# Performance work log

Hardware: AMD Instinct MI355X
Metric: run time of the kernel (lower is better)

Reference implementation:

```python
import jax, jax.numpy as jnp
import numpy as np

EMBED_DIM = 1024
NUM_HEADS = 16
HEAD_DIM = EMBED_DIM // NUM_HEADS


def setup_inputs() -> dict:
    key = jax.random.key(0)
    ks = jax.random.split(key, 9)
    B, S, E = 2, 2048, EMBED_DIM
    scale = 1.0 / np.sqrt(E)
    return {
        "query": jax.random.normal(ks[0], (B, S, E), jnp.float32),
        "key": jax.random.normal(ks[1], (B, S, E), jnp.float32),
        "value": jax.random.normal(ks[2], (B, S, E), jnp.float32),
        "wq": jax.random.normal(ks[3], (E, E), jnp.float32) * scale,
        "bq": jnp.zeros((E,), jnp.float32),
        "wk": jax.random.normal(ks[4], (E, E), jnp.float32) * scale,
        "bk": jnp.zeros((E,), jnp.float32),
        "wv": jax.random.normal(ks[5], (E, E), jnp.float32) * scale,
        "bv": jnp.zeros((E,), jnp.float32),
    }


def _split_heads(x):
    B, S, _ = x.shape
    return x.reshape(B, S, NUM_HEADS, HEAD_DIM).transpose(0, 2, 1, 3)  # [B,H,S,Dh]


def reference(query, key, value, wq, bq, wk, bk, wv, bv):
    q = _split_heads(query @ wq + bq)   # [B,H,S,Dh]
    k = _split_heads(key @ wk + bk)
    v = _split_heads(value @ wv + bv)
    logits = jnp.einsum("bhqd,bhkd->bhqk", q, k) / jnp.sqrt(
        jnp.asarray(HEAD_DIM, q.dtype)
    )
    attn = jax.nn.softmax(logits, axis=-1)          # [B,H,S,S]
    out = jnp.einsum("bhqk,bhkd->bhqd", attn, v)    # [B,H,S,Dh]
    B, H, S, Dh = out.shape
    out = out.transpose(0, 2, 1, 3).reshape(B, S, H * Dh)  # [B,S,E]
    return out, attn
```

## Files before the change

### kernel.cpp

```cpp
#include <hip/hip_runtime.h>

typedef float  f32x4   __attribute__((ext_vector_type(4)));
typedef float  f32x16  __attribute__((ext_vector_type(16)));
typedef int    i32x4   __attribute__((ext_vector_type(4)));
typedef short  bf16x8  __attribute__((ext_vector_type(8)));
typedef short  s16x4   __attribute__((ext_vector_type(4)));

#define NB   2
#define SEQ  2048
#define EMB  1024
#define NH   16
#define DH   64
#define MATN (NB * SEQ * EMB)

__device__ inline short f2bf(float f) {
    unsigned u = __float_as_uint(f);
    u += 0x7fffu + ((u >> 16) & 1u);
    return (short)(u >> 16);
}

__device__ inline unsigned cvtpk(float lo, float hi) {
    unsigned r;
    asm("v_cvt_pk_bf16_f32 %0, %1, %2" : "=v"(r) : "v"(lo), "v"(hi));
    return r;
}

__device__ inline float fexp2(float x) {
#if __has_builtin(__builtin_amdgcn_exp2f)
    return __builtin_amdgcn_exp2f(x);
#else
    return exp2f(x);
#endif
}

__device__ inline f32x4 mfma16(bf16x8 a, bf16x8 b, f32x4 c) {
    return __builtin_amdgcn_mfma_f32_16x16x32_bf16(a, b, c, 0, 0, 0);
}
__device__ inline f32x16 mfma32(bf16x8 a, bf16x8 b, f32x16 c) {
    return __builtin_amdgcn_mfma_f32_32x32x16_bf16(a, b, c, 0, 0, 0);
}

__device__ inline void gload_lds16(const short* g, short* l) {
    __builtin_amdgcn_global_load_lds(
        (const __attribute__((address_space(1))) void*)g,
        (__attribute__((address_space(3))) void*)l, 16, 0, 0);
}

__global__ __launch_bounds__(256) void prep_kernel(const float* __restrict__ q,
                                                   const float* __restrict__ k,
                                                   const float* __restrict__ v,
                                                   const float* __restrict__ w0,
                                                   const float* __restrict__ w1,
                                                   const float* __restrict__ w2,
                                                   short* __restrict__ wt,
                                                   short* __restrict__ abf) {
    int blk = blockIdx.x;
    int t = threadIdx.x;
    if (blk < 3072) {
        __shared__ float tile[32][33];
        int mat = blk >> 10;
        int rem = blk & 1023;
        int kt = rem >> 5, nt = rem & 31;
        const float* W = (mat == 0) ? w0 : ((mat == 1) ? w1 : w2);
        int row = t >> 3, c4 = (t & 7) << 2;

        f32x4 val = *(const f32x4*)(W + (kt * 32 + row) * EMB + nt * 32 + c4);
        tile[row][c4 + 0] = val[0];
        tile[row][c4 + 1] = val[1];
        tile[row][c4 + 2] = val[2];
        tile[row][c4 + 3] = val[3];
        __syncthreads();

        int n = nt * 32 + row;
        s16x4 o;
        o[0] = f2bf(tile[c4 + 0][row]);
        o[1] = f2bf(tile[c4 + 1][row]);
        o[2] = f2bf(tile[c4 + 2][row]);
        o[3] = f2bf(tile[c4 + 3][row]);
        *(s16x4*)(wt + mat * (EMB * EMB) + n * EMB + kt * 32 + c4) = o;
    } else {
        long long i = (long long)(blk - 3072) * 2048 + t * 8;
        int mat = (int)(i >> 22);
        int off = (int)(i & (MATN - 1));
        const float* A = (mat == 0) ? q : ((mat == 1) ? k : v);
        f32x4 x = *(const f32x4*)(A + off);
        f32x4 y = *(const f32x4*)(A + off + 4);
        bf16x8 pk;
        pk[0] = f2bf(x[0]); pk[1] = f2bf(x[1]); pk[2] = f2bf(x[2]); pk[3] = f2bf(x[3]);
        pk[4] = f2bf(y[0]); pk[5] = f2bf(y[1]); pk[6] = f2bf(y[2]); pk[7] = f2bf(y[3]);
        *(bf16x8*)(abf + i) = pk;
    }
}

template <bool BF16A>
__global__ __launch_bounds__(256) void proj_kernel(const short* __restrict__ abf,
                                                   const float* __restrict__ a0,
                                                   const float* __restrict__ a1,
                                                   const float* __restrict__ a2,
                                                   const float* __restrict__ b0,
                                                   const float* __restrict__ b1,
                                                   const float* __restrict__ b2,
                                                   const short* __restrict__ wt,
                                                   short* __restrict__ qkv) {
    __shared__ __align__(16) short smem[18432];

    int orig = blockIdx.x;
    int blk = (orig & 7) * 96 + (orig >> 3);
    int mat = blk >> 8;
    int rem = blk & 255;
    int mt = rem >> 3, nt = rem & 7;

    const float* bias = (mat == 0) ? b0 : ((mat == 1) ? b1 : b2);
    const float* Af = (mat == 0) ? a0 : ((mat == 1) ? a1 : a2);
    const short* Ab = abf + mat * MATN;
    const short* WT = wt + mat * (EMB * EMB);
    short* O = qkv + mat * MATN;
    float scale = (mat == 0) ? 0.125f * 1.44269504f : 1.0f;

    int t = threadIdx.x;
    int lane = t & 63, w = t >> 6;
    int wr = w >> 1, wc = w & 1;
    int lg = lane >> 4, lm = lane & 15;

    int m0 = mt * 128, n0 = nt * 128;

    f32x4 acc[4][4] = {};

    if constexpr (BF16A) {
        const short* gA[4];
        const short* gW[4];
        int ldso[4];
#pragma unroll
        for (int i = 0; i < 4; i++) {
            int u = w * 256 + i * 64 + lane;
            int row = u >> 3;
            int c = (u & 7) ^ (row & 7);
            gA[i] = Ab + (m0 + row) * EMB + c * 8;
            gW[i] = WT + (n0 + row) * EMB + c * 8;
            ldso[i] = (w * 256 + i * 64) * 8;
        }
        int xr = lm & 7;
        for (int k0 = 0; k0 < EMB; k0 += 64) {
#pragma unroll
            for (int i = 0; i < 4; i++) {
                gload_lds16(gA[i] + k0, smem + ldso[i]);
                gload_lds16(gW[i] + k0, smem + 8192 + ldso[i]);
            }
            __syncthreads();
#pragma unroll
            for (int ks = 0; ks < 2; ks++) {
                bf16x8 af[4], bfr[4];
                int cc = (ks * 4 + lg) ^ xr;
#pragma unroll
                for (int mi = 0; mi < 4; mi++)
                    af[mi] = *(const bf16x8*)(smem + (wr * 64 + mi * 16 + lm) * 64 + cc * 8);
#pragma unroll
                for (int ni = 0; ni < 4; ni++)
                    bfr[ni] = *(const bf16x8*)(smem + 8192 + (wc * 64 + ni * 16 + lm) * 64 + cc * 8);
#pragma unroll
                for (int mi = 0; mi < 4; mi++)
#pragma unroll
                    for (int ni = 0; ni < 4; ni++)
                        acc[mi][ni] = mfma16(af[mi], bfr[ni], acc[mi][ni]);
            }
            __syncthreads();
        }
    } else {
        int srow = t >> 1, koff = (t & 1) * 32;
        for (int k0 = 0; k0 < EMB; k0 += 64) {
            const float* ap = Af + (m0 + srow) * EMB + k0 + koff;
#pragma unroll
            for (int i = 0; i < 4; i++) {
                f32x4 x = *(const f32x4*)(ap + i * 8);
                f32x4 y = *(const f32x4*)(ap + i * 8 + 4);
                bf16x8 pk;
                pk[0] = f2bf(x[0]); pk[1] = f2bf(x[1]); pk[2] = f2bf(x[2]); pk[3] = f2bf(x[3]);
                pk[4] = f2bf(y[0]); pk[5] = f2bf(y[1]); pk[6] = f2bf(y[2]); pk[7] = f2bf(y[3]);
                *(bf16x8*)&smem[srow * 72 + koff + i * 8] = pk;
            }
            const short* wp = WT + (n0 + srow) * EMB + k0 + koff;
#pragma unroll
            for (int i = 0; i < 4; i++)
                *(i32x4*)&smem[9216 + srow * 72 + koff + i * 8] = *(const i32x4*)(wp + i * 8);
            __syncthreads();
#pragma unroll
            for (int ks = 0; ks < 2; ks++) {
                bf16x8 af[4], bfr[4];
#pragma unroll
                for (int mi = 0; mi < 4; mi++)
                    af[mi] = *(const bf16x8*)&smem[(wr * 64 + mi * 16 + lm) * 72 + ks * 32 + lg * 8];
#pragma unroll
                for (int ni = 0; ni < 4; ni++)
                    bfr[ni] = *(const bf16x8*)&smem[9216 + (wc * 64 + ni * 16 + lm) * 72 + ks * 32 + lg * 8];
#pragma unroll
                for (int mi = 0; mi < 4; mi++)
#pragma unroll
                    for (int ni = 0; ni < 4; ni++)
                        acc[mi][ni] = mfma16(af[mi], bfr[ni], acc[mi][ni]);
            }
            __syncthreads();
        }
    }

    int bidx = m0 >> 11;
    if (mat == 2) {
#pragma unroll
        for (int ni = 0; ni < 4; ni++) {
            int e = n0 + wc * 64 + ni * 16 + lm;
            float bv = bias[e];
            int h = e >> 6, d = e & 63;
#pragma unroll
            for (int mi = 0; mi < 4; mi++) {
                int s = (m0 + wr * 64 + mi * 16 + lg * 4) & (SEQ - 1);
                s16x4 o;
#pragma unroll
                for (int r = 0; r < 4; r++) o[r] = f2bf(acc[mi][ni][r] + bv);
                *(s16x4*)(O + (((bidx * NH + h) * DH + d) * SEQ) + s) = o;
            }
        }
    } else {
#pragma unroll
        for (int ni = 0; ni < 4; ni++) {
            int e = n0 + wc * 64 + ni * 16 + lm;
            float bv = bias[e];
#pragma unroll
            for (int mi = 0; mi < 4; mi++) {
                int rr = wr * 64 + mi * 16 + lg * 4;
#pragma unroll
                for (int r = 0; r < 4; r++)
                    smem[(rr + r) * 136 + wc * 64 + ni * 16 + lm] =
                        f2bf((acc[mi][ni][r] + bv) * scale);
            }
        }
        __syncthreads();
        int r = t >> 1, half = t & 1;
        int h = (n0 + half * 64) >> 6;
        int s = (m0 + r) & (SEQ - 1);
        short* dst = O + (((long long)bidx * NH + h) * SEQ + s) * DH;
        const short* srcp = smem + r * 136 + half * 64;
#pragma unroll
        for (int j = 0; j < 8; j++)
            *(i32x4*)(dst + j * 8) = *(const i32x4*)(srcp + j * 8);
    }
}

__global__ __launch_bounds__(256) void attn_kernel(const short* __restrict__ qkv,
                                                   float* __restrict__ out,
                                                   float* __restrict__ attn) {
    const short* Qb = qkv;
    const short* Kb = qkv + MATN;
    const short* Vt = qkv + 2 * MATN;

    __shared__ __align__(16) short kbuf[2][64][72];
    __shared__ __align__(16) short vbuf[2][4096];
    __shared__ float lds_rs[4][32];

    int orig = blockIdx.x;
    int wg = (orig & 7) * 128 + (orig >> 3);
    int bh = wg >> 5;
    int q0 = (wg & 31) * 64;
    int b = bh >> 4, hq = bh & 15;

    int t = threadIdx.x, lane = t & 63, w = t >> 6;
    int srow = t >> 2, sch = t & 3;
    int l31 = lane & 31, l5 = lane >> 5;
    int qh = w & 1, kh = w >> 1;

    const short* kbase = Kb + (long long)bh * SEQ * DH;
    const short* vbase = Vt + (long long)bh * DH * SEQ;

    bf16x8 qw[4];
    {
        const short* qr = Qb + ((long long)bh * SEQ + q0 + qh * 32 + l31) * DH + l5 * 8;
        qw[0] = *(const bf16x8*)(qr);
        qw[1] = *(const bf16x8*)(qr + 16);
        qw[2] = *(const bf16x8*)(qr + 32);
        qw[3] = *(const bf16x8*)(qr + 48);
    }

    i32x4 kr0, kr1;
    {
        const short* kp = kbase + srow * DH + sch * 16;
        kr0 = *(const i32x4*)(kp); kr1 = *(const i32x4*)(kp + 8);
    }
    float rsum = 0.0f;
    for (int kt = 0; kt < 32; kt++) {
        *(i32x4*)&kbuf[kt & 1][srow][sch * 16]     = kr0;
        *(i32x4*)&kbuf[kt & 1][srow][sch * 16 + 8] = kr1;
        __syncthreads();
        if (kt < 31) {
            const short* kp = kbase + ((kt + 1) * 64 + srow) * DH + sch * 16;
            kr0 = *(const i32x4*)(kp); kr1 = *(const i32x4*)(kp + 8);
        }
        const short* kb = &kbuf[kt & 1][kh * 32 + l31][l5 * 8];
        f32x16 s = {};
        __builtin_amdgcn_s_setprio(1);
        s = mfma32(*(const bf16x8*)(kb),      qw[0], s);
        s = mfma32(*(const bf16x8*)(kb + 16), qw[1], s);
        s = mfma32(*(const bf16x8*)(kb + 32), qw[2], s);
        s = mfma32(*(const bf16x8*)(kb + 48), qw[3], s);
        __builtin_amdgcn_s_setprio(0);
#pragma unroll
        for (int r = 0; r < 16; r++) rsum += fexp2(s[r]);
    }
    rsum += __shfl_xor(rsum, 32);
    if (lane < 32) lds_rs[w][lane] = rsum;
    __syncthreads();
    float ml2r = -__log2f(lds_rs[qh][l31] + lds_rs[2 + qh][l31]);

    f32x16 acc2[2] = {};
    float* arow2 = attn + ((long long)bh * SEQ + q0 + qh * 32 + l31) * SEQ + kh * 32;

    int vidx = ((sch >> 1) * 2 + (sch & 1)) * 2 + (srow >> 5);
    int vA = vidx * 512 + (srow & 31) * 8;

    i32x4 vr0, vr1;
    {
        const short* kp = kbase + srow * DH + sch * 16;
        kr0 = *(const i32x4*)(kp); kr1 = *(const i32x4*)(kp + 8);
        const short* vp = vbase + srow * SEQ + sch * 16;
        vr0 = *(const i32x4*)(vp); vr1 = *(const i32x4*)(vp + 8);
    }

    for (int kt = 0; kt < 32; kt++) {
        *(i32x4*)&kbuf[kt & 1][srow][sch * 16]     = kr0;
        *(i32x4*)&kbuf[kt & 1][srow][sch * 16 + 8] = kr1;
        union { i32x4 v; s16x4 h[2]; } u0, u1;
        u0.v = vr0; u1.v = vr1;
        *(s16x4*)&vbuf[kt & 1][vA]       = u0.h[0];
        *(s16x4*)&vbuf[kt & 1][vA + 256] = u0.h[1];
        *(s16x4*)&vbuf[kt & 1][vA + 4]   = u1.h[0];
        *(s16x4*)&vbuf[kt & 1][vA + 260] = u1.h[1];
        __syncthreads();
        if (kt < 31) {
            const short* kp = kbase + ((kt + 1) * 64 + srow) * DH + sch * 16;
            kr0 = *(const i32x4*)(kp); kr1 = *(const i32x4*)(kp + 8);
            const short* vp = vbase + srow * SEQ + (kt + 1) * 64 + sch * 16;
            vr0 = *(const i32x4*)(vp); vr1 = *(const i32x4*)(vp + 8);
        }

        const short* kb2 = &kbuf[kt & 1][kh * 32 + l31][l5 * 8];
        f32x16 s;
#pragma unroll
        for (int r = 0; r < 16; r++) s[r] = ml2r;
        __builtin_amdgcn_s_setprio(1);
        s = mfma32(*(const bf16x8*)(kb2),      qw[0], s);
        s = mfma32(*(const bf16x8*)(kb2 + 16), qw[1], s);
        s = mfma32(*(const bf16x8*)(kb2 + 32), qw[2], s);
        s = mfma32(*(const bf16x8*)(kb2 + 48), qw[3], s);
        __builtin_amdgcn_s_setprio(0);

        float p[16];
#pragma unroll
        for (int rg = 0; rg < 4; rg++) {
            f32x4 st;
#pragma unroll
            for (int j = 0; j < 4; j++) {
                float e = fexp2(s[rg * 4 + j]);
                p[rg * 4 + j] = e;
                st[j] = e;
            }
            *(f32x4*)(arow2 + kt * 64 + rg * 8 + l5 * 4) = st;
        }

        bf16x8 pb[2];
#pragma unroll
        for (int c = 0; c < 2; c++) {
            union { unsigned d[4]; bf16x8 v; } up;
            up.d[0] = cvtpk(p[c * 8 + 0], p[c * 8 + 1]);
            up.d[1] = cvtpk(p[c * 8 + 2], p[c * 8 + 3]);
            up.d[2] = cvtpk(p[c * 8 + 4], p[c * 8 + 5]);
            up.d[3] = cvtpk(p[c * 8 + 6], p[c * 8 + 7]);
            pb[c] = up.v;
        }

        __builtin_amdgcn_s_setprio(1);
#pragma unroll
        for (int db = 0; db < 2; db++) {
#pragma unroll
            for (int c = 0; c < 2; c++) {
                bf16x8 vf = *(const bf16x8*)&vbuf[kt & 1]
                    [((kh * 2 + c) * 2 + db) * 512 + l5 * 256 + l31 * 8];
                acc2[db] = mfma32(vf, pb[c], acc2[db]);
            }
        }
        __builtin_amdgcn_s_setprio(0);
    }

    __syncthreads();
    float* mrg = (float*)&kbuf[0][0][0];
    if (kh == 1) {
#pragma unroll
        for (int db = 0; db < 2; db++)
#pragma unroll
            for (int rg = 0; rg < 4; rg++) {
                f32x4 v = {acc2[db][rg * 4 + 0], acc2[db][rg * 4 + 1],
                           acc2[db][rg * 4 + 2], acc2[db][rg * 4 + 3]};
                *(f32x4*)&mrg[((qh * 2 + db) * 4 + rg) * 256 + lane * 4] = v;
            }
    }
    __syncthreads();
    if (kh == 0) {
        float* op2 = out + ((long long)b * SEQ + q0 + qh * 32 + l31) * EMB + hq * DH;
#pragma unroll
        for (int db = 0; db < 2; db++)
#pragma unroll
            for (int rg = 0; rg < 4; rg++) {
                f32x4 m = *(const f32x4*)&mrg[((qh * 2 + db) * 4 + rg) * 256 + lane * 4];
                f32x4 o = {acc2[db][rg * 4 + 0] + m[0], acc2[db][rg * 4 + 1] + m[1],
                           acc2[db][rg * 4 + 2] + m[2], acc2[db][rg * 4 + 3] + m[3]};
                *(f32x4*)(op2 + db * 32 + rg * 8 + l5 * 4) = o;
            }
    }
}

extern "C" void kernel_launch(void* const* d_in, const int* in_sizes, int n_in,
                              void* d_out, int out_size, void* d_ws, size_t ws_size,
                              hipStream_t stream) {
    const float* query = (const float*)d_in[0];
    const float* key   = (const float*)d_in[1];
    const float* value = (const float*)d_in[2];
    const float* wq    = (const float*)d_in[3];
    const float* bq    = (const float*)d_in[4];
    const float* wk    = (const float*)d_in[5];
    const float* bk    = (const float*)d_in[6];
    const float* wv    = (const float*)d_in[7];
    const float* bv    = (const float*)d_in[8];

    float* out  = (float*)d_out;
    float* attn = out + (long long)NB * SEQ * EMB;

    size_t need_full = ((size_t)3 * EMB * EMB + 6ull * MATN) * sizeof(short);
    bool bf16a = ws_size >= need_full;

    short* wt  = (short*)d_ws;
    short* abf = wt + 3 * (EMB * EMB);
    short* qkv = bf16a ? (abf + 3 * MATN) : abf;

    hipLaunchKernelGGL(prep_kernel, dim3(bf16a ? 9216 : 3072), dim3(256), 0, stream,
                       query, key, value, wq, wk, wv, wt, abf);
    if (bf16a) {
        hipLaunchKernelGGL((proj_kernel<true>), dim3(768), dim3(256), 0, stream,
                           abf, query, key, value, bq, bk, bv, wt, qkv);
    } else {
        hipLaunchKernelGGL((proj_kernel<false>), dim3(768), dim3(256), 0, stream,
                           abf, query, key, value, bq, bk, bv, wt, qkv);
    }
    hipLaunchKernelGGL(attn_kernel, dim3(1024), dim3(256), 0, stream,
                       qkv, out, attn);
}
```

Before: 268.6 us.

## Give each attention wave its own 32 queries across all keys; swizzle K LDS

The attention workgroup now covers 128 queries instead of 64, and each wave owns 32 query rows and handles both 32-key halves of each tile. This removes the cross-wave split-K reduction through LDS and the extra syncs at the end. Each K/V tile loaded into LDS is now reused by twice as many queries, and the grid is halved. The K buffer uses an XOR swizzle instead of padding to avoid bank conflicts. The trade-off is fewer workgroups, which lowers occupancy and parallelism on the GPU, and more serial work per wave.

After: 250.6 us. -6.7%, faster.

```diff
diff --git a/kernel.cpp b/kernel.cpp
--- a/kernel.cpp
+++ b/kernel.cpp
@@ -251,27 +251,34 @@
     const short* Kb = qkv + MATN;
     const short* Vt = qkv + 2 * MATN;
 
-    __shared__ __align__(16) short kbuf[2][64][72];
+    __shared__ __align__(16) short kbuf[2][4096];
     __shared__ __align__(16) short vbuf[2][4096];
-    __shared__ float lds_rs[4][32];
+    float* lds_rs = (float*)&vbuf[0][0];
 
     int orig = blockIdx.x;
-    int wg = (orig & 7) * 128 + (orig >> 3);
-    int bh = wg >> 5;
-    int q0 = (wg & 31) * 64;
+    int wg = (orig & 7) * 64 + (orig >> 3);
+    int bh = wg >> 4;
+    int q0 = (wg & 15) * 128;
     int b = bh >> 4, hq = bh & 15;
 
     int t = threadIdx.x, lane = t & 63, w = t >> 6;
     int srow = t >> 2, sch = t & 3;
     int l31 = lane & 31, l5 = lane >> 5;
-    int qh = w & 1, kh = w >> 1;
 
     const short* kbase = Kb + (long long)bh * SEQ * DH;
     const short* vbase = Vt + (long long)bh * DH * SEQ;
 
+    int kc0 = ((sch * 2)     ^ (srow & 7)) * 8;
+    int kc1 = ((sch * 2 + 1) ^ (srow & 7)) * 8;
+    int xr1 = l31 & 7;
+    int ko0 = ((l5    ) ^ xr1) * 8;
+    int ko1 = ((l5 + 2) ^ xr1) * 8;
+    int ko2 = ((l5 + 4) ^ xr1) * 8;
+    int ko3 = ((l5 + 6) ^ xr1) * 8;
+
     bf16x8 qw[4];
     {
-        const short* qr = Qb + ((long long)bh * SEQ + q0 + qh * 32 + l31) * DH + l5 * 8;
+        const short* qr = Qb + ((long long)bh * SEQ + q0 + w * 32 + l31) * DH + l5 * 8;
         qw[0] = *(const bf16x8*)(qr);
         qw[1] = *(const bf16x8*)(qr + 16);
         qw[2] = *(const bf16x8*)(qr + 32);
@@ -285,34 +292,37 @@
     }
     float rsum = 0.0f;
     for (int kt = 0; kt < 32; kt++) {
-        *(i32x4*)&kbuf[kt & 1][srow][sch * 16]     = kr0;
-        *(i32x4*)&kbuf[kt & 1][srow][sch * 16 + 8] = kr1;
+        *(i32x4*)&kbuf[kt & 1][srow * 64 + kc0] = kr0;
+        *(i32x4*)&kbuf[kt & 1][srow * 64 + kc1] = kr1;
         __syncthreads();
         if (kt < 31) {
             const short* kp = kbase + ((kt + 1) * 64 + srow) * DH + sch * 16;
             kr0 = *(const i32x4*)(kp); kr1 = *(const i32x4*)(kp + 8);
         }
-        const short* kb = &kbuf[kt & 1][kh * 32 + l31][l5 * 8];
-        f32x16 s = {};
-        __builtin_amdgcn_s_setprio(1);
-        s = mfma32(*(const bf16x8*)(kb),      qw[0], s);
-        s = mfma32(*(const bf16x8*)(kb + 16), qw[1], s);
-        s = mfma32(*(const bf16x8*)(kb + 32), qw[2], s);
-        s = mfma32(*(const bf16x8*)(kb + 48), qw[3], s);
-        __builtin_amdgcn_s_setprio(0);
-#pragma unroll
-        for (int r = 0; r < 16; r++) rsum += fexp2(s[r]);
+#pragma unroll
+        for (int kb = 0; kb < 2; kb++) {
+            const short* kp2 = &kbuf[kt & 1][(kb * 32 + l31) * 64];
+            f32x16 s = {};
+            __builtin_amdgcn_s_setprio(1);
+            s = mfma32(*(const bf16x8*)(kp2 + ko0), qw[0], s);
+            s = mfma32(*(const bf16x8*)(kp2 + ko1), qw[1], s);
+            s = mfma32(*(const bf16x8*)(kp2 + ko2), qw[2], s);
+            s = mfma32(*(const bf16x8*)(kp2 + ko3), qw[3], s);
+            __builtin_amdgcn_s_setprio(0);
+#pragma unroll
+            for (int r = 0; r < 16; r++) rsum += fexp2(s[r]);
+        }
     }
     rsum += __shfl_xor(rsum, 32);
-    if (lane < 32) lds_rs[w][lane] = rsum;
+    if (lane < 32) lds_rs[w * 32 + lane] = rsum;
     __syncthreads();
-    float ml2r = -__log2f(lds_rs[qh][l31] + lds_rs[2 + qh][l31]);
+    float ml2r = -__log2f(lds_rs[w * 32 + l31]);
+    __syncthreads();
 
     f32x16 acc2[2] = {};
-    float* arow2 = attn + ((long long)bh * SEQ + q0 + qh * 32 + l31) * SEQ + kh * 32;
-
-    int vidx = ((sch >> 1) * 2 + (sch & 1)) * 2 + (srow >> 5);
-    int vA = vidx * 512 + (srow & 31) * 8;
+    float* arow = attn + ((long long)bh * SEQ + q0 + w * 32 + l31) * SEQ;
+
+    int vA = (sch * 2 + (srow >> 5)) * 512 + (srow & 31) * 8;
 
     i32x4 vr0, vr1;
     {
@@ -323,8 +333,8 @@
     }
 
     for (int kt = 0; kt < 32; kt++) {
-        *(i32x4*)&kbuf[kt & 1][srow][sch * 16]     = kr0;
-        *(i32x4*)&kbuf[kt & 1][srow][sch * 16 + 8] = kr1;
+        *(i32x4*)&kbuf[kt & 1][srow * 64 + kc0] = kr0;
+        *(i32x4*)&kbuf[kt & 1][srow * 64 + kc1] = kr1;
         union { i32x4 v; s16x4 h[2]; } u0, u1;
         u0.v = vr0; u1.v = vr1;
         *(s16x4*)&vbuf[kt & 1][vA]       = u0.h[0];
@@ -339,79 +349,66 @@
             vr0 = *(const i32x4*)(vp); vr1 = *(const i32x4*)(vp + 8);
         }
 
-        const short* kb2 = &kbuf[kt & 1][kh * 32 + l31][l5 * 8];
-        f32x16 s;
-#pragma unroll
-        for (int r = 0; r < 16; r++) s[r] = ml2r;
-        __builtin_amdgcn_s_setprio(1);
-        s = mfma32(*(const bf16x8*)(kb2),      qw[0], s);
-        s = mfma32(*(const bf16x8*)(kb2 + 16), qw[1], s);
-        s = mfma32(*(const bf16x8*)(kb2 + 32), qw[2], s);
-        s = mfma32(*(const bf16x8*)(kb2 + 48), qw[3], s);
-        __builtin_amdgcn_s_setprio(0);
-
-        float p[16];
+#pragma unroll
+        for (int kb = 0; kb < 2; kb++) {
+            const short* kp2 = &kbuf[kt & 1][(kb * 32 + l31) * 64];
+            f32x16 s;
+#pragma unroll
+            for (int r = 0; r < 16; r++) s[r] = ml2r;
+            __builtin_amdgcn_s_setprio(1);
+            s = mfma32(*(const bf16x8*)(kp2 + ko0), qw[0], s);
+            s = mfma32(*(const bf16x8*)(kp2 + ko1), qw[1], s);
+            s = mfma32(*(const bf16x8*)(kp2 + ko2), qw[2], s);
+            s = mfma32(*(const bf16x8*)(kp2 + ko3), qw[3], s);
+            __builtin_amdgcn_s_setprio(0);
+
+            float p[16];
+#pragma unroll
+            for (int rg = 0; rg < 4; rg++) {
+                f32x4 st;
+#pragma unroll
+                for (int j = 0; j < 4; j++) {
+                    float e = fexp2(s[rg * 4 + j]);
+                    p[rg * 4 + j] = e;
+                    st[j] = e;
+                }
+                *(f32x4*)(arow + kt * 64 + kb * 32 + rg * 8 + l5 * 4) = st;
+            }
+
+            bf16x8 pb[2];
+#pragma unroll
+            for (int f = 0; f < 2; f++) {
+                union { unsigned d[4]; bf16x8 v; } up;
+                up.d[0] = cvtpk(p[f * 8 + 0], p[f * 8 + 1]);
+                up.d[1] = cvtpk(p[f * 8 + 2], p[f * 8 + 3]);
+                up.d[2] = cvtpk(p[f * 8 + 4], p[f * 8 + 5]);
+                up.d[3] = cvtpk(p[f * 8 + 6], p[f * 8 + 7]);
+                pb[f] = up.v;
+            }
+
+            __builtin_amdgcn_s_setprio(1);
+#pragma unroll
+            for (int db = 0; db < 2; db++) {
+#pragma unroll
+                for (int f = 0; f < 2; f++) {
+                    bf16x8 vf = *(const bf16x8*)&vbuf[kt & 1]
+                        [((kb * 2 + f) * 2 + db) * 512 + l5 * 256 + l31 * 8];
+                    acc2[db] = mfma32(vf, pb[f], acc2[db]);
+                }
+            }
+            __builtin_amdgcn_s_setprio(0);
+        }
+    }
+
+    float* op = out + ((long long)b * SEQ + q0 + w * 32 + l31) * EMB + hq * DH;
+#pragma unroll
+    for (int db = 0; db < 2; db++)
 #pragma unroll
         for (int rg = 0; rg < 4; rg++) {
-            f32x4 st;
-#pragma unroll
-            for (int j = 0; j < 4; j++) {
-                float e = fexp2(s[rg * 4 + j]);
-                p[rg * 4 + j] = e;
-                st[j] = e;
-            }
-            *(f32x4*)(arow2 + kt * 64 + rg * 8 + l5 * 4) = st;
-        }
-
-        bf16x8 pb[2];
-#pragma unroll
-        for (int c = 0; c < 2; c++) {
-            union { unsigned d[4]; bf16x8 v; } up;
-            up.d[0] = cvtpk(p[c * 8 + 0], p[c * 8 + 1]);
-            up.d[1] = cvtpk(p[c * 8 + 2], p[c * 8 + 3]);
-            up.d[2] = cvtpk(p[c * 8 + 4], p[c * 8 + 5]);
-            up.d[3] = cvtpk(p[c * 8 + 6], p[c * 8 + 7]);
-            pb[c] = up.v;
-        }
-
-        __builtin_amdgcn_s_setprio(1);
-#pragma unroll
-        for (int db = 0; db < 2; db++) {
-#pragma unroll
-            for (int c = 0; c < 2; c++) {
-                bf16x8 vf = *(const bf16x8*)&vbuf[kt & 1]
-                    [((kh * 2 + c) * 2 + db) * 512 + l5 * 256 + l31 * 8];
-                acc2[db] = mfma32(vf, pb[c], acc2[db]);
-            }
-        }
-        __builtin_amdgcn_s_setprio(0);
-    }
-
-    __syncthreads();
-    float* mrg = (float*)&kbuf[0][0][0];
-    if (kh == 1) {
-#pragma unroll
-        for (int db = 0; db < 2; db++)
-#pragma unroll
-            for (int rg = 0; rg < 4; rg++) {
-                f32x4 v = {acc2[db][rg * 4 + 0], acc2[db][rg * 4 + 1],
-                           acc2[db][rg * 4 + 2], acc2[db][rg * 4 + 3]};
-                *(f32x4*)&mrg[((qh * 2 + db) * 4 + rg) * 256 + lane * 4] = v;
-            }
-    }
-    __syncthreads();
-    if (kh == 0) {
-        float* op2 = out + ((long long)b * SEQ + q0 + qh * 32 + l31) * EMB + hq * DH;
-#pragma unroll
-        for (int db = 0; db < 2; db++)
-#pragma unroll
-            for (int rg = 0; rg < 4; rg++) {
-                f32x4 m = *(const f32x4*)&mrg[((qh * 2 + db) * 4 + rg) * 256 + lane * 4];
-                f32x4 o = {acc2[db][rg * 4 + 0] + m[0], acc2[db][rg * 4 + 1] + m[1],
-                           acc2[db][rg * 4 + 2] + m[2], acc2[db][rg * 4 + 3] + m[3]};
-                *(f32x4*)(op2 + db * 32 + rg * 8 + l5 * 4) = o;
-            }
-    }
+            f32x4 o = {acc2[db][rg * 4 + 0], acc2[db][rg * 4 + 1],
+                       acc2[db][rg * 4 + 2], acc2[db][rg * 4 + 3]};
+            *(f32x4*)(op + db * 32 + rg * 8 + l5 * 4) = o;
+        }
 }
 
 extern "C" void kernel_launch(void* const* d_in, const int* in_sizes, int n_in,
@@ -446,6 +443,6 @@
         hipLaunchKernelGGL((proj_kernel<false>), dim3(768), dim3(256), 0, stream,
                            abf, query, key, value, bq, bk, bv, wt, qkv);
     }
-    hipLaunchKernelGGL(attn_kernel, dim3(1024), dim3(256), 0, stream,
+    hipLaunchKernelGGL(attn_kernel, dim3(512), dim3(256), 0, stream,
                        qkv, out, attn);
 }
```
